# Performance work log

Measured on AMD Instinct MI355X. Metric: run time of the kernel, lower is better.

## Reference

```python
import jax, jax.numpy as jnp
import numpy as np

N_NODES = 50000
N_EDGES = 800000
IN_C, HID_C, OUT_C = 256, 256, 128


def gcn_conv(x, W, b, row, col, n_nodes):
    """PyG GCNConv: linear transform, symmetric-normalized aggregation, bias.
    row/col already include self-loops. Messages flow row -> col."""
    h = x @ W  # [N, out]
    deg = jax.ops.segment_sum(jnp.ones_like(col, dtype=h.dtype), col, num_segments=n_nodes)
    d_inv_sqrt = jnp.where(deg > 0, jax.lax.rsqrt(jnp.maximum(deg, 1e-12)), 0.0)
    norm = d_inv_sqrt[row] * d_inv_sqrt[col]  # [E]
    msg = h[row] * norm[:, None]              # gather + scale, [E, out]
    out = jax.ops.segment_sum(msg, col, num_segments=n_nodes)  # scatter-add
    return out + b


def setup_inputs() -> dict:
    key = jax.random.key(0)
    k_x, k_e, k_w1, k_w2 = jax.random.split(key, 4)
    x = jax.random.normal(k_x, (N_NODES, IN_C), dtype=jnp.float32)
    edge_index = jax.random.randint(k_e, (2, N_EDGES), 0, N_NODES, dtype=jnp.int64)
    # Glorot-style init for GCN weights, zeros bias (PyG default)
    s1 = float(np.sqrt(6.0 / (IN_C + HID_C)))
    s2 = float(np.sqrt(6.0 / (HID_C + OUT_C)))
    W1 = jax.random.uniform(k_w1, (IN_C, HID_C), dtype=jnp.float32, minval=-s1, maxval=s1)
    b1 = jnp.zeros((HID_C,), dtype=jnp.float32)
    W2 = jax.random.uniform(k_w2, (HID_C, OUT_C), dtype=jnp.float32, minval=-s2, maxval=s2)
    b2 = jnp.zeros((OUT_C,), dtype=jnp.float32)
    return {"x": x, "edge_index": edge_index, "W1": W1, "b1": b1, "W2": W2, "b2": b2}


def reference(x, edge_index, W1, b1, W2, b2):
    n = x.shape[0]
    # add self-loops (PyG GCNConv default add_self_loops=True)
    loops = jnp.arange(n, dtype=edge_index.dtype)
    row = jnp.concatenate([edge_index[0], loops])
    col = jnp.concatenate([edge_index[1], loops])
    h = gcn_conv(x, W1, b1, row, col, n)
    h = jax.nn.relu(h)  # dropout p=0.0 -> identity
    out = gcn_conv(h, W2, b2, row, col, n)
    return out
```

## Files before the change

### kernel.cpp

```cpp
#include <hip/hip_runtime.h>

#define NN 50000
#define NE 800000
#define IN_C 256
#define HID_C 256
#define OUT_C 128

#define NET (NE + NN)
#define NBUCK 196
#define CHUNK 4096
#define NPA 196
#define CAP_B 5120

typedef unsigned short u16;
typedef unsigned int u32;
typedef __attribute__((ext_vector_type(8))) short short8;
typedef __attribute__((ext_vector_type(8))) unsigned short ushort8;
typedef __attribute__((ext_vector_type(4))) float f32x4;
typedef __attribute__((ext_vector_type(2))) float f32x2;
typedef __attribute__((ext_vector_type(4))) unsigned u32x4;
typedef __attribute__((ext_vector_type(4), aligned(4))) unsigned u32x4u;

#define CPS ((size_t)(NN + 1) * 32)

__device__ __forceinline__ u16 f2b(float f) {
  unsigned int u = __float_as_uint(f);
  return (u16)((u + 0x7FFFu + ((u >> 16) & 1u)) >> 16);
}
__device__ __forceinline__ float b2f(u16 s) {
  return __uint_as_float(((unsigned int)s) << 16);
}


__global__ __launch_bounds__(256) void convw_zero(const float* __restrict__ W1,
                                                  const float* __restrict__ W2,
                                                  u16* __restrict__ W1t,
                                                  u16* __restrict__ W2t,
                                                  int* __restrict__ cnt,
                                                  u16* __restrict__ Hb,
                                                  int nzb) {
  int b = blockIdx.x;
  if (b < 256) {
    int id = b * 256 + threadIdx.x;
    if (id < 256 * 256) {
      int n = id >> 8, k = id & 255;
      W1t[id] = f2b(W1[k * 256 + n]);
    }
    if (id < 128 * 256) {
      int n = id >> 8, k = id & 255;
      W2t[id] = f2b(W2[k * 128 + n]);
    }
  } else if (b < 256 + nzb) {
    int i = (b - 256) * 256 + threadIdx.x;
    if (i < NN) cnt[i] = 1;
  } else {
    int t = threadIdx.x;
    Hb[(size_t)(t >> 5) * CPS + (size_t)NN * 32 + (t & 31)] = 0;
  }
}


__global__ __launch_bounds__(256) void hist_kernel(const int* __restrict__ col,
                                                   int* __restrict__ cnt, int E) {
  int e = blockIdx.x * blockDim.x + threadIdx.x;
  if (e < E) atomicAdd(&cnt[col[e]], 1);
}

__global__ __launch_bounds__(256) void scan1_kernel(const int* __restrict__ cnt,
                                                    int* __restrict__ bsum, int n) {
  __shared__ int ws[4];
  int i = blockIdx.x * 256 + threadIdx.x;
  int lane = threadIdx.x & 63, wid = threadIdx.x >> 6;
  int v = (i < n) ? cnt[i] : 0;
#pragma unroll
  for (int off = 32; off > 0; off >>= 1) v += __shfl_down(v, off, 64);
  if (lane == 0) ws[wid] = v;
  __syncthreads();
  if (threadIdx.x == 0) bsum[blockIdx.x] = ws[0] + ws[1] + ws[2] + ws[3];
}

__global__ __launch_bounds__(256) void scan2_kernel(const int* __restrict__ bsum,
                                                    int* __restrict__ boff,
                                                    int* __restrict__ row_off,
                                                    int nb, int n) {
  __shared__ int wsum[4], wpre[5];
  int lane = threadIdx.x & 63, wid = threadIdx.x >> 6;
  int v = (threadIdx.x < nb) ? bsum[threadIdx.x] : 0;
  int s = v;
#pragma unroll
  for (int off = 1; off < 64; off <<= 1) {
    int t = __shfl_up(s, off, 64);
    if (lane >= off) s += t;
  }
  if (lane == 63) wsum[wid] = s;
  __syncthreads();
  if (threadIdx.x == 0) {
    int acc = 0;
#pragma unroll
    for (int w = 0; w < 4; ++w) { wpre[w] = acc; acc += wsum[w]; }
    wpre[4] = acc;
  }
  __syncthreads();
  if (threadIdx.x < nb) boff[threadIdx.x] = wpre[wid] + (s - v);
  if (threadIdx.x == 0) row_off[n] = wpre[4];
}

__global__ __launch_bounds__(256) void scan3_kernel(const int* __restrict__ cnt,
                                                    const int* __restrict__ boff,
                                                    int* __restrict__ row_off,
                                                    int* __restrict__ bcur,
                                                    float* __restrict__ dinv, int n) {
  __shared__ int wsum[4], wpre[4];
  int i = blockIdx.x * 256 + threadIdx.x;
  int lane = threadIdx.x & 63, wid = threadIdx.x >> 6;
  int v = (i < n) ? cnt[i] : 0;
  int s = v;
#pragma unroll
  for (int off = 1; off < 64; off <<= 1) {
    int t = __shfl_up(s, off, 64);
    if (lane >= off) s += t;
  }
  if (lane == 63) wsum[wid] = s;
  __syncthreads();
  if (threadIdx.x == 0) {
    int acc = 0;
#pragma unroll
    for (int w = 0; w < 4; ++w) { wpre[w] = acc; acc += wsum[w]; }
  }
  __syncthreads();
  if (i < n) {
    int off = boff[blockIdx.x] + wpre[wid] + (s - v);
    row_off[i] = off;
    if ((i & 255) == 0) bcur[i >> 8] = off;
    dinv[i] = rsqrtf((float)v);
  }
}


template <bool A_IS_F32, bool PLANAR_C>
__device__ __forceinline__ void gemm_body(const void* __restrict__ Ap,
                                          const u16* __restrict__ Bt,
                                          const float* __restrict__ dscale,
                                          u16* __restrict__ C, int M, int N,
                                          int bx, int by,
                                          u16 (&Asl)[2][5120], u16 (&Bsl)[2][5120]) {
  const int tid = threadIdx.x;
  const int row0 = by * 128;
  const int col0 = bx * 128;

  f32x4 acc[4][4] = {};

  const int seg = tid & 7;
  const int rb = tid >> 3;
  const int wave = tid >> 6, lane = tid & 63;
  const int wm = wave >> 1, wn = wave & 1;
  const int qr = lane & 15, quad = lane >> 4;

  float4 aF[4];
  ushort4 aU[4];
  ushort4 bR[4];

  auto load_tiles = [&](int k0) {
    if constexpr (A_IS_F32) {
      const float* A = (const float*)Ap;
#pragma unroll
      for (int i = 0; i < 4; ++i) {
        int gr = row0 + rb + i * 32;
        aF[i] = (gr < M) ? *(const float4*)&A[(size_t)gr * 256 + k0 + seg * 4]
                         : make_float4(0.f, 0.f, 0.f, 0.f);
      }
    } else {
      const u16* A = (const u16*)Ap;
#pragma unroll
      for (int i = 0; i < 4; ++i) {
        int gr = row0 + rb + i * 32;
        aU[i] = (gr < M) ? *(const ushort4*)&A[(size_t)gr * 256 + k0 + seg * 4]
                         : make_ushort4(0, 0, 0, 0);
      }
    }
#pragma unroll
    for (int i = 0; i < 4; ++i) {
      int n = rb + i * 32;
      bR[i] = *(const ushort4*)&Bt[(size_t)(col0 + n) * 256 + k0 + seg * 4];
    }
  };

  auto write_lds = [&](int buf) {
#pragma unroll
    for (int i = 0; i < 4; ++i) {
      int r = rb + i * 32;
      ushort4 u;
      if constexpr (A_IS_F32) {
        u.x = f2b(aF[i].x); u.y = f2b(aF[i].y);
        u.z = f2b(aF[i].z); u.w = f2b(aF[i].w);
      } else {
        u = aU[i];
      }
      *(ushort4*)&Asl[buf][r * 40 + seg * 4] = u;
      *(ushort4*)&Bsl[buf][r * 40 + seg * 4] = bR[i];
    }
  };

  load_tiles(0);
  write_lds(0);
  __syncthreads();

#pragma unroll
  for (int it = 0; it < 8; ++it) {
    const int cur = it & 1;
    if (it < 7) load_tiles((it + 1) * 32);

    short8 afr[4], bfr[4];
#pragma unroll
    for (int mt = 0; mt < 4; ++mt)
      afr[mt] = *(const short8*)&Asl[cur][(wm * 64 + mt * 16 + qr) * 40 + quad * 8];
#pragma unroll
    for (int nt = 0; nt < 4; ++nt)
      bfr[nt] = *(const short8*)&Bsl[cur][(wn * 64 + nt * 16 + qr) * 40 + quad * 8];
#pragma unroll
    for (int mt = 0; mt < 4; ++mt)
#pragma unroll
      for (int nt = 0; nt < 4; ++nt)
        acc[mt][nt] = __builtin_amdgcn_mfma_f32_16x16x32_bf16(afr[mt], bfr[nt], acc[mt][nt], 0, 0, 0);

    if (it < 7) {
      write_lds(1 - cur);
      __syncthreads();
    }
  }

#pragma unroll
  for (int mt = 0; mt < 4; ++mt) {
#pragma unroll
    for (int i = 0; i < 4; ++i) {
      int gr = row0 + wm * 64 + mt * 16 + quad * 4 + i;
      if (gr < M) {
        float sc = dscale[gr];
#pragma unroll
        for (int nt = 0; nt < 4; ++nt) {
          int gc = col0 + wn * 64 + nt * 16 + qr;
          u16 val = f2b(acc[mt][nt][i] * sc);
          if constexpr (PLANAR_C)
            C[(size_t)(gc >> 5) * CPS + (size_t)gr * 32 + (gc & 31)] = val;
          else
            C[(size_t)gr * N + gc] = val;
        }
      }
    }
  }
}

template <bool A_IS_F32, bool PLANAR_C>
__global__ __launch_bounds__(256) void gemm_mfma(const void* __restrict__ Ap,
                                                 const u16* __restrict__ Bt,
                                                 const float* __restrict__ dscale,
                                                 u16* __restrict__ C, int M, int N,
                                                 u16* __restrict__ zrow) {
  if (zrow != nullptr && blockIdx.x == 0 && blockIdx.y == 0 && threadIdx.x < 128) {
    int t = threadIdx.x;
    zrow[(size_t)(t >> 5) * CPS + (size_t)NN * 32 + (t & 31)] = 0;
  }
  __shared__ u16 Asl[2][5120];
  __shared__ u16 Bsl[2][5120];
  gemm_body<A_IS_F32, PLANAR_C>(Ap, Bt, dscale, C, M, N, blockIdx.x, blockIdx.y, Asl, Bsl);
}

__global__ __launch_bounds__(256) void gemm1_scatter(const float* __restrict__ x,
                                                     const u16* __restrict__ W1t,
                                                     const float* __restrict__ dinv,
                                                     u16* __restrict__ Hb, int M, int N,
                                                     int ngb,
                                                     const int* __restrict__ row,
                                                     const int* __restrict__ col,
                                                     int* __restrict__ bcur,
                                                     uint2* __restrict__ stage, int E) {
  __shared__ u16 ABsl[4][5120];
  int b = blockIdx.x;
  if (b < ngb) {
    gemm_body<true, true>(x, W1t, dinv, Hb, M, N, b & 1, b >> 1,
                          *reinterpret_cast<u16(*)[2][5120]>(&ABsl[0]),
                          *reinterpret_cast<u16(*)[2][5120]>(&ABsl[2]));
  } else {
    uint2* pairs = (uint2*)ABsl;
    int* hcnt = (int*)((char*)ABsl + 32768);
    int* hscan = hcnt + 256;
    int* hbase = hscan + 256;
    int* lcur = hbase + 256;

    const int tid = threadIdx.x;
    const int blk = b - ngb;
    const int e0 = blk * CHUNK;

    hcnt[tid] = 0;
    __syncthreads();

    int ecol[16], erow[16];
#pragma unroll
    for (int j = 0; j < 16; ++j) {
      int e = e0 + j * 256 + tid;
      if (e < E) {
        ecol[j] = col[e];
        erow[j] = row[e];
        atomicAdd(&hcnt[ecol[j] >> 8], 1);
      } else {
        ecol[j] = -1;
      }
    }
    __syncthreads();

    hscan[tid] = hcnt[tid];
    __syncthreads();
#pragma unroll
    for (int off = 1; off < 256; off <<= 1) {
      int t = (tid >= off) ? hscan[tid - off] : 0;
      __syncthreads();
      hscan[tid] += t;
      __syncthreads();
    }

    lcur[tid] = 0;
    if (hcnt[tid] > 0) hbase[tid] = atomicAdd(&bcur[tid], hcnt[tid]);
    __syncthreads();

#pragma unroll
    for (int j = 0; j < 16; ++j) {
      if (ecol[j] >= 0) {
        int bk = ecol[j] >> 8;
        int p = atomicAdd(&lcur[bk], 1);
        pairs[(hscan[bk] - hcnt[bk]) + p] = make_uint2((unsigned)erow[j], (unsigned)ecol[j]);
      }
    }
    __syncthreads();

    int mtot = hscan[255];
    for (int s = tid; s < mtot; s += 256) {
      uint2 pr = pairs[s];
      int bk = (int)(pr.y >> 8);
      stage[hbase[bk] + (s - (hscan[bk] - hcnt[bk]))] = pr;
    }
  }
}

__global__ __launch_bounds__(256) void csr_sort(const uint2* __restrict__ stage,
                                                const int* __restrict__ row_off,
                                                u32* __restrict__ csrp) {
  __shared__ int cur[256];
  __shared__ u32 outb[CAP_B];
  const int b = blockIdx.x;
  const int base_node = b << 8;
  const int nnodes = min(256, NN - base_node);
  const int tid = threadIdx.x;
  const int bstart = row_off[base_node];
  const int bend = row_off[min(base_node + 256, NN)];
  if (tid < nnodes) {
    int c0 = row_off[base_node + tid] - bstart;
    outb[c0] = (u32)(base_node + tid);
    cur[tid] = c0 + 1;
  }
  __syncthreads();
  const int m = bend - bstart;
  const int mreal = m - nnodes;
  for (int i = tid; i < mreal; i += 256) {
    uint2 pr = stage[bstart + i];
    int cl = ((int)pr.y - base_node) & 255;
    int p = atomicAdd(&cur[cl], 1);
    u32 val = pr.x & 0xFFFFu;
    if (p < CAP_B) outb[p] = val;
    else if (bstart + p < NET) csrp[bstart + p] = val;
  }
  __syncthreads();
  const int mm = min(m, CAP_B);
  for (int i = tid; i < mm; i += 256) csrp[bstart + i] = outb[i];
}

template <int NPL, int OUTC, bool RELU_BF16>
__global__ __launch_bounds__(256) void agg_gather(const u16* __restrict__ h,
                                                  const int* __restrict__ row_off,
                                                  const u32* __restrict__ csrp,
                                                  const float* __restrict__ dinv,
                                                  const float* __restrict__ bias,
                                                  void* __restrict__ outp) {
  const int slice = blockIdx.x % NPL;
  const int wave = threadIdx.x >> 6;
  const int lane = threadIdx.x & 63;
  const int nd = lane >> 2;
  const int c = lane & 3;
  const int v = (blockIdx.x / NPL) * 64 + wave * 16 + nd;
  if (v >= NN) return;
  const u16* hpl = h + (size_t)slice * CPS;
  const int beg = row_off[v], end = row_off[v + 1];
  const int coff = c * 8;

  f32x2 a0 = {}, a1 = {}, a2 = {}, a3 = {};
  for (int p = beg; p < end; p += 8) {
    u32x4u cwa = *(const u32x4u*)&csrp[p];
    u32x4u cwb = *(const u32x4u*)&csrp[p + 4];
    unsigned s0 = (p + 0 < end) ? (cwa[0] & 0xFFFFu) : (unsigned)NN;
    unsigned s1 = (p + 1 < end) ? (cwa[1] & 0xFFFFu) : (unsigned)NN;
    unsigned s2 = (p + 2 < end) ? (cwa[2] & 0xFFFFu) : (unsigned)NN;
    unsigned s3 = (p + 3 < end) ? (cwa[3] & 0xFFFFu) : (unsigned)NN;
    unsigned s4 = (p + 4 < end) ? (cwb[0] & 0xFFFFu) : (unsigned)NN;
    unsigned s5 = (p + 5 < end) ? (cwb[1] & 0xFFFFu) : (unsigned)NN;
    unsigned s6 = (p + 6 < end) ? (cwb[2] & 0xFFFFu) : (unsigned)NN;
    unsigned s7 = (p + 7 < end) ? (cwb[3] & 0xFFFFu) : (unsigned)NN;
    u32x4 g0 = *(const u32x4*)&hpl[(size_t)s0 * 32 + coff];
    u32x4 g1 = *(const u32x4*)&hpl[(size_t)s1 * 32 + coff];
    u32x4 g2 = *(const u32x4*)&hpl[(size_t)s2 * 32 + coff];
    u32x4 g3 = *(const u32x4*)&hpl[(size_t)s3 * 32 + coff];
    u32x4 g4 = *(const u32x4*)&hpl[(size_t)s4 * 32 + coff];
    u32x4 g5 = *(const u32x4*)&hpl[(size_t)s5 * 32 + coff];
    u32x4 g6 = *(const u32x4*)&hpl[(size_t)s6 * 32 + coff];
    u32x4 g7 = *(const u32x4*)&hpl[(size_t)s7 * 32 + coff];
#pragma unroll
    for (int q = 0; q < 4; ++q) {
      f32x2 t;
      f32x2 acc = {};
      t[0] = __uint_as_float(g0[q] << 16); t[1] = __uint_as_float(g0[q] & 0xffff0000u); acc += t;
      t[0] = __uint_as_float(g1[q] << 16); t[1] = __uint_as_float(g1[q] & 0xffff0000u); acc += t;
      t[0] = __uint_as_float(g2[q] << 16); t[1] = __uint_as_float(g2[q] & 0xffff0000u); acc += t;
      t[0] = __uint_as_float(g3[q] << 16); t[1] = __uint_as_float(g3[q] & 0xffff0000u); acc += t;
      t[0] = __uint_as_float(g4[q] << 16); t[1] = __uint_as_float(g4[q] & 0xffff0000u); acc += t;
      t[0] = __uint_as_float(g5[q] << 16); t[1] = __uint_as_float(g5[q] & 0xffff0000u); acc += t;
      t[0] = __uint_as_float(g6[q] << 16); t[1] = __uint_as_float(g6[q] & 0xffff0000u); acc += t;
      t[0] = __uint_as_float(g7[q] << 16); t[1] = __uint_as_float(g7[q] & 0xffff0000u); acc += t;
      if (q == 0) a0 += acc;
      else if (q == 1) a1 += acc;
      else if (q == 2) a2 += acc;
      else a3 += acc;
    }
  }
  float aa[8] = {a0[0], a0[1], a1[0], a1[1], a2[0], a2[1], a3[0], a3[1]};
  const int cg = slice * 32 + coff;
  float dv = dinv[v];
  float4 bv0 = *(const float4*)&bias[cg];
  float4 bv1 = *(const float4*)&bias[cg + 4];
  float bb[8] = {bv0.x, bv0.y, bv0.z, bv0.w, bv1.x, bv1.y, bv1.z, bv1.w};
  if constexpr (RELU_BF16) {
    u16* o = (u16*)outp;
    ushort8 ov;
#pragma unroll
    for (int i = 0; i < 8; ++i) ov[i] = (short)f2b(fmaxf(aa[i] * dv + bb[i], 0.f));
    *(ushort8*)&o[(size_t)v * OUTC + cg] = ov;
  } else {
    float* o = (float*)outp;
    float ov[8];
#pragma unroll
    for (int i = 0; i < 8; ++i) ov[i] = aa[i] * dv + bb[i];
    *(float4*)&o[(size_t)v * OUTC + cg] = make_float4(ov[0], ov[1], ov[2], ov[3]);
    *(float4*)&o[(size_t)v * OUTC + cg + 4] = make_float4(ov[4], ov[5], ov[6], ov[7]);
  }
}


extern "C" void kernel_launch(void* const* d_in, const int* in_sizes, int n_in,
                              void* d_out, int out_size, void* d_ws, size_t ws_size,
                              hipStream_t stream) {
  const float* x = (const float*)d_in[0];
  const int* ei = (const int*)d_in[1];
  const float* W1 = (const float*)d_in[2];
  const float* b1 = (const float*)d_in[3];
  const float* W2 = (const float*)d_in[4];
  const float* b2 = (const float*)d_in[5];
  float* out = (float*)d_out;

  const int* row = ei;
  const int* col = ei + NE;

  const int NB = (NN + 255) / 256;

  u16* Hb = (u16*)d_ws;
  u16* H2b = Hb + (size_t)(NN + 1) * 256;
  u16* H3b = H2b + (size_t)NN * 256;
  u16* W1t = H3b + (size_t)(NN + 1) * 128;
  u16* W2t = W1t + 256 * 256;
  int* cnt = (int*)(W2t + 128 * 256);
  int* row_off = cnt + NN;
  int* bcur = row_off + NN + 4;
  float* dinv = (float*)(bcur + 256);
  int* bsum = (int*)(dinv + NN);
  int* boff = bsum + 200;
  u32* csrp = (u32*)(boff + 200);
  uint2* stage = (uint2*)H3b;

  convw_zero<<<256 + NB + 1, 256, 0, stream>>>(W1, W2, W1t, W2t, cnt, Hb, NB);
  hist_kernel<<<(NE + 255) / 256, 256, 0, stream>>>(col, cnt, NE);
  scan1_kernel<<<NB, 256, 0, stream>>>(cnt, bsum, NN);
  scan2_kernel<<<1, 256, 0, stream>>>(bsum, boff, row_off, NB, NN);
  scan3_kernel<<<NB, 256, 0, stream>>>(cnt, boff, row_off, bcur, dinv, NN);

  {
    const int ngb = (HID_C / 128) * ((NN + 127) / 128);
    gemm1_scatter<<<ngb + NPA, 256, 0, stream>>>(x, W1t, dinv, Hb, NN, HID_C, ngb,
                                                 row, col, bcur, stage, NE);
  }
  csr_sort<<<NBUCK, 256, 0, stream>>>(stage, row_off, csrp);

  const int NGB = (NN + 63) / 64;
  agg_gather<8, 256, true><<<NGB * 8, 256, 0, stream>>>(
      Hb, row_off, csrp, dinv, b1, H2b);

  {
    dim3 grid(OUT_C / 128, (NN + 127) / 128);
    gemm_mfma<false, true><<<grid, 256, 0, stream>>>(H2b, W2t, dinv, H3b, NN, OUT_C, H3b);
  }

  agg_gather<4, 128, false><<<NGB * 4, 256, 0, stream>>>(
      H3b, row_off, csrp, dinv, b2, out);
}
```

Measured before the change: 268.1 us.

## Pad CSR rows to multiples of eight with u16 indices and prefetch

Rounds each node's CSR segment up to a multiple of 8, filling the padding with the dummy zero row NN. The aggregation loop can then drop the per-element bounds checks. Column indices are stored as u16 instead of u32, which halves index traffic, and the next 8 indices are prefetched one iteration ahead. The cost is up to 7 extra padded gathers per node, which each read the zero row, plus extra fill work in csr_sort. Correctness relies on node ids fitting in 16 bits and on bcur holding the per-bucket real-edge end after the scatter.

```diff
diff --git a/kernel.cpp b/kernel.cpp
--- a/kernel.cpp
+++ b/kernel.cpp
@@ -6,11 +6,11 @@
 #define HID_C 256
 #define OUT_C 128
 
-#define NET (NE + NN)
+#define NETP (NE + 8 * NN)
 #define NBUCK 196
 #define CHUNK 4096
 #define NPA 196
-#define CAP_B 5120
+#define CAP_B 6400
 
 typedef unsigned short u16;
 typedef unsigned int u32;
@@ -19,7 +19,6 @@
 typedef __attribute__((ext_vector_type(4))) float f32x4;
 typedef __attribute__((ext_vector_type(2))) float f32x2;
 typedef __attribute__((ext_vector_type(4))) unsigned u32x4;
-typedef __attribute__((ext_vector_type(4), aligned(4))) unsigned u32x4u;
 
 #define CPS ((size_t)(NN + 1) * 32)
 
@@ -71,7 +70,7 @@
   __shared__ int ws[4];
   int i = blockIdx.x * 256 + threadIdx.x;
   int lane = threadIdx.x & 63, wid = threadIdx.x >> 6;
-  int v = (i < n) ? cnt[i] : 0;
+  int v = (i < n) ? ((cnt[i] + 7) & ~7) : 0;
 #pragma unroll
   for (int off = 32; off > 0; off >>= 1) v += __shfl_down(v, off, 64);
   if (lane == 0) ws[wid] = v;
@@ -113,7 +112,8 @@
   __shared__ int wsum[4], wpre[4];
   int i = blockIdx.x * 256 + threadIdx.x;
   int lane = threadIdx.x & 63, wid = threadIdx.x >> 6;
-  int v = (i < n) ? cnt[i] : 0;
+  int vr = (i < n) ? cnt[i] : 0;
+  int v = (vr + 7) & ~7;
   int s = v;
 #pragma unroll
   for (int off = 1; off < 64; off <<= 1) {
@@ -132,7 +132,7 @@
     int off = boff[blockIdx.x] + wpre[wid] + (s - v);
     row_off[i] = off;
     if ((i & 255) == 0) bcur[i >> 8] = off;
-    dinv[i] = rsqrtf((float)v);
+    dinv[i] = rsqrtf((float)vr);
   }
 }
 
@@ -343,40 +343,43 @@
 
 __global__ __launch_bounds__(256) void csr_sort(const uint2* __restrict__ stage,
                                                 const int* __restrict__ row_off,
-                                                u32* __restrict__ csrp) {
+                                                const int* __restrict__ bcur,
+                                                u16* __restrict__ csrp) {
   __shared__ int cur[256];
-  __shared__ u32 outb[CAP_B];
+  __shared__ u16 outb[CAP_B];
   const int b = blockIdx.x;
   const int base_node = b << 8;
   const int nnodes = min(256, NN - base_node);
   const int tid = threadIdx.x;
   const int bstart = row_off[base_node];
   const int bend = row_off[min(base_node + 256, NN)];
+  const int m = bend - bstart;
+  const int mm = min(m, CAP_B);
+  for (int i = tid; i < mm; i += 256) outb[i] = (u16)NN;
+  for (int i = CAP_B + tid; i < m; i += 256) csrp[bstart + i] = (u16)NN;
+  __syncthreads();
   if (tid < nnodes) {
     int c0 = row_off[base_node + tid] - bstart;
-    outb[c0] = (u32)(base_node + tid);
+    outb[c0] = (u16)(base_node + tid);
     cur[tid] = c0 + 1;
   }
   __syncthreads();
-  const int m = bend - bstart;
-  const int mreal = m - nnodes;
+  const int mreal = bcur[b] - bstart - 0;
   for (int i = tid; i < mreal; i += 256) {
     uint2 pr = stage[bstart + i];
     int cl = ((int)pr.y - base_node) & 255;
     int p = atomicAdd(&cur[cl], 1);
-    u32 val = pr.x & 0xFFFFu;
-    if (p < CAP_B) outb[p] = val;
-    else if (bstart + p < NET) csrp[bstart + p] = val;
-  }
-  __syncthreads();
-  const int mm = min(m, CAP_B);
+    if (p < CAP_B) outb[p] = (u16)pr.x;
+    else if (bstart + p < NETP) csrp[bstart + p] = (u16)pr.x;
+  }
+  __syncthreads();
   for (int i = tid; i < mm; i += 256) csrp[bstart + i] = outb[i];
 }
 
 template <int NPL, int OUTC, bool RELU_BF16>
 __global__ __launch_bounds__(256) void agg_gather(const u16* __restrict__ h,
                                                   const int* __restrict__ row_off,
-                                                  const u32* __restrict__ csrp,
+                                                  const u16* __restrict__ csrp,
                                                   const float* __restrict__ dinv,
                                                   const float* __restrict__ bias,
                                                   void* __restrict__ outp) {
@@ -392,25 +395,17 @@
   const int coff = c * 8;
 
   f32x2 a0 = {}, a1 = {}, a2 = {}, a3 = {};
+  ushort8 cwA = *(const ushort8*)&csrp[beg];
   for (int p = beg; p < end; p += 8) {
-    u32x4u cwa = *(const u32x4u*)&csrp[p];
-    u32x4u cwb = *(const u32x4u*)&csrp[p + 4];
-    unsigned s0 = (p + 0 < end) ? (cwa[0] & 0xFFFFu) : (unsigned)NN;
-    unsigned s1 = (p + 1 < end) ? (cwa[1] & 0xFFFFu) : (unsigned)NN;
-    unsigned s2 = (p + 2 < end) ? (cwa[2] & 0xFFFFu) : (unsigned)NN;
-    unsigned s3 = (p + 3 < end) ? (cwa[3] & 0xFFFFu) : (unsigned)NN;
-    unsigned s4 = (p + 4 < end) ? (cwb[0] & 0xFFFFu) : (unsigned)NN;
-    unsigned s5 = (p + 5 < end) ? (cwb[1] & 0xFFFFu) : (unsigned)NN;
-    unsigned s6 = (p + 6 < end) ? (cwb[2] & 0xFFFFu) : (unsigned)NN;
-    unsigned s7 = (p + 7 < end) ? (cwb[3] & 0xFFFFu) : (unsigned)NN;
-    u32x4 g0 = *(const u32x4*)&hpl[(size_t)s0 * 32 + coff];
-    u32x4 g1 = *(const u32x4*)&hpl[(size_t)s1 * 32 + coff];
-    u32x4 g2 = *(const u32x4*)&hpl[(size_t)s2 * 32 + coff];
-    u32x4 g3 = *(const u32x4*)&hpl[(size_t)s3 * 32 + coff];
-    u32x4 g4 = *(const u32x4*)&hpl[(size_t)s4 * 32 + coff];
-    u32x4 g5 = *(const u32x4*)&hpl[(size_t)s5 * 32 + coff];
-    u32x4 g6 = *(const u32x4*)&hpl[(size_t)s6 * 32 + coff];
-    u32x4 g7 = *(const u32x4*)&hpl[(size_t)s7 * 32 + coff];
+    ushort8 cwB = *(const ushort8*)&csrp[p + 8];
+    u32x4 g0 = *(const u32x4*)&hpl[(size_t)cwA[0] * 32 + coff];
+    u32x4 g1 = *(const u32x4*)&hpl[(size_t)cwA[1] * 32 + coff];
+    u32x4 g2 = *(const u32x4*)&hpl[(size_t)cwA[2] * 32 + coff];
+    u32x4 g3 = *(const u32x4*)&hpl[(size_t)cwA[3] * 32 + coff];
+    u32x4 g4 = *(const u32x4*)&hpl[(size_t)cwA[4] * 32 + coff];
+    u32x4 g5 = *(const u32x4*)&hpl[(size_t)cwA[5] * 32 + coff];
+    u32x4 g6 = *(const u32x4*)&hpl[(size_t)cwA[6] * 32 + coff];
+    u32x4 g7 = *(const u32x4*)&hpl[(size_t)cwA[7] * 32 + coff];
 #pragma unroll
     for (int q = 0; q < 4; ++q) {
       f32x2 t;
@@ -428,6 +423,7 @@
       else if (q == 2) a2 += acc;
       else a3 += acc;
     }
+    cwA = cwB;
   }
   float aa[8] = {a0[0], a0[1], a1[0], a1[1], a2[0], a2[1], a3[0], a3[1]};
   const int cg = slice * 32 + coff;
@@ -479,7 +475,7 @@
   float* dinv = (float*)(bcur + 256);
   int* bsum = (int*)(dinv + NN);
   int* boff = bsum + 200;
-  u32* csrp = (u32*)(boff + 200);
+  u16* csrp = (u16*)(boff + 200);
   uint2* stage = (uint2*)H3b;
 
   convw_zero<<<256 + NB + 1, 256, 0, stream>>>(W1, W2, W1t, W2t, cnt, Hb, NB);
@@ -493,7 +489,7 @@
     gemm1_scatter<<<ngb + NPA, 256, 0, stream>>>(x, W1t, dinv, Hb, NN, HID_C, ngb,
                                                  row, col, bcur, stage, NE);
   }
-  csr_sort<<<NBUCK, 256, 0, stream>>>(stage, row_off, csrp);
+  csr_sort<<<NBUCK, 256, 0, stream>>>(stage, row_off, bcur, csrp);
 
   const int NGB = (NN + 63) / 64;
   agg_gather<8, 256, true><<<NGB * 8, 256, 0, stream>>>(
```

New measurement: 262.1 us. 2.3% less time.
